# Performance work log

Measured on AMD Instinct MI355X. Metric: run time of the kernel, lower is better.

## Reference

```python
import jax, jax.numpy as jnp
import numpy as np

B, D, H = 16384, 1024, 4096


def setup_inputs() -> dict:
    key = jax.random.key(0)
    kx, kp, k1, k2 = jax.random.split(key, 4)
    X = jax.random.normal(kx, (B, D), dtype=jnp.float32)
    prot_col_idx = 3
    # protected column must be binary {0,1} so the remap produces no NaNs
    prot = jax.random.randint(kp, (B,), 0, 2).astype(jnp.float32)
    X = X.at[:, prot_col_idx].set(prot)
    W1 = jax.random.normal(k1, (D, H), dtype=jnp.float32) * (1.0 / np.sqrt(D))
    b1 = jnp.zeros((H,), dtype=jnp.float32)
    W2 = jax.random.normal(k2, (H, D), dtype=jnp.float32) * (1.0 / np.sqrt(H))
    b2 = jnp.zeros((D,), dtype=jnp.float32)
    return {"X": X, "W1": W1, "b1": b1, "W2": W2, "b2": b2,
            "prot_col_idx": prot_col_idx}


def reference(X, W1, b1, W2, b2, prot_col_idx):
    def explainer(x):
        h = jnp.tanh(x @ W1 + b1)          # [B, H]
        return h @ W2 + b2                  # [B, D]

    # vectorized remap of the protected column: 0 -> 1, 1 -> 0, else NaN
    col = X[:, prot_col_idx]
    flipped = jnp.where(col == 0, jnp.float32(1.0),
                        jnp.where(col == 1, jnp.float32(0.0), jnp.float32(jnp.nan)))
    X_copy = X.at[:, prot_col_idx].set(flipped.astype(X.dtype))

    shaps = explainer(X)
    shaps_counter = explainer(X_copy)
    mean_euclid_dist = jnp.mean(jnp.abs(shaps - shaps_counter), axis=0)  # [D]
    return mean_euclid_dist.sum()
```

## Files before the change

### kernel.cpp

```cpp
#include <hip/hip_runtime.h>
#include <stdint.h>

#define B_N 16384
#define D_N 1024
#define H_N 4096

typedef int i32x4 __attribute__((ext_vector_type(4)));
typedef int i32x8 __attribute__((ext_vector_type(8)));
typedef float f32x4 __attribute__((ext_vector_type(4)));

__device__ __forceinline__ void gload16(const void* g, void* l) {
  __builtin_amdgcn_global_load_lds((const __attribute__((address_space(1))) void*)g,
                                   (__attribute__((address_space(3))) void*)l,
                                   16, 0, 0);
}

__device__ __forceinline__ unsigned char f2fp8(float v) {
  return (unsigned char)(__builtin_amdgcn_cvt_pk_fp8_f32(v, v, 0, false) & 0xFF);
}

__device__ __forceinline__ int perm_h(int h) {
  return (h & ~63) | ((h & 15) << 2) | ((h >> 4) & 3);
}

__device__ __forceinline__ void transpose_tile(
    const float* __restrict__ in, unsigned char* __restrict__ out,
    int R, int C, float scale, float* __restrict__ w3, int pci,
    int i0, int j0, int tx, int ty, bool permute) {
  __shared__ float tile[32][33];
#pragma unroll
  for (int r = 0; r < 32; r += 8) {
    int i = i0 + ty + r;
    int j = j0 + tx;
    float v = in[(size_t)i * C + j];
    tile[ty + r][tx] = v;
    if (w3 != nullptr && i == pci) w3[j] = v;
  }
  __syncthreads();
#pragma unroll
  for (int r = 0; r < 32; r += 8) {
    int jo = j0 + ty + r;
    int io = i0 + tx;
    int ioo = permute ? perm_h(io) : io;
    out[(size_t)jo * R + ioo] = f2fp8(tile[tx][ty + r] * scale);
  }
}

__global__ __launch_bounds__(256) void prep_kernel(
    const float4* __restrict__ X4, int* __restrict__ Xb,
    float* __restrict__ s,
    const float* __restrict__ W1, unsigned char* __restrict__ W1T, float* __restrict__ w3,
    const float* __restrict__ W2, unsigned char* __restrict__ W2T,
    const int* __restrict__ pci_p, float* __restrict__ out0) {
  int b = blockIdx.x;
  int tid = threadIdx.x;
  int pci = *pci_p;
  if (b == 0 && tid == 0) out0[0] = 0.0f;
  if (b < 8192) {
    int i = (b * 256 + tid) * 2;
#pragma unroll
    for (int u = 0; u < 2; u++) {
      float4 v = X4[i + u];
      int p = __builtin_amdgcn_cvt_pk_fp8_f32(v.x, v.y, 0, false);
      p = __builtin_amdgcn_cvt_pk_fp8_f32(v.z, v.w, p, true);
      Xb[i + u] = p;
      if (((i + u) & (D_N / 4 - 1)) == (pci >> 2)) {
        int row = (i + u) >> 8;
        float c;
        switch (pci & 3) {
          case 0:  c = v.x; break;
          case 1:  c = v.y; break;
          case 2:  c = v.z; break;
          default: c = v.w; break;
        }
        s[row] = 1.0f - 2.0f * c;
      }
    }
  } else if (b < 12288) {
    int id = b - 8192;
    transpose_tile(W1, W1T, D_N, H_N, 16.0f, w3, pci,
                   (id >> 7) * 32, (id & 127) * 32, tid & 31, tid >> 5, false);
  } else {
    int id = b - 12288;
    transpose_tile(W2, W2T, H_N, D_N, 64.0f, nullptr, -1,
                   (id >> 5) * 32, (id & 31) * 32, tid & 31, tid >> 5, true);
  }
}

template <int KTOT>
__device__ __forceinline__ void mx_mainloop(
    const unsigned char* __restrict__ A, const unsigned char* __restrict__ B,
    int m0, int n0, int sa, int sb,
    unsigned char* As, unsigned char* Bs, f32x4 (&acc)[4][4]) {
  const int tid = threadIdx.x;
  const int lane = tid & 63;
  const int wave = tid >> 6;
  const int wm = (wave >> 1) * 64;
  const int wn = (wave & 1) * 64;
  const int lm = lane & 15;
  const int quad = lane >> 4;

  const int srow = tid >> 3;
  const int clog = (tid & 7) ^ (srow & 7);
  const unsigned char* Ag = A + (size_t)(m0 + srow) * KTOT + clog * 16;
  const unsigned char* Bg = B + (size_t)(n0 + srow) * KTOT + clog * 16;
  unsigned char* As_l = As + tid * 16;
  unsigned char* Bs_l = Bs + tid * 16;

  for (int k0 = 0; k0 < KTOT; k0 += 128) {
#pragma unroll
    for (int it = 0; it < 4; it++) {
      gload16(Ag + k0 + (size_t)(32 * it) * KTOT, As_l + it * 4096);
      gload16(Bg + k0 + (size_t)(32 * it) * KTOT, Bs_l + it * 4096);
    }
    __syncthreads();
    i32x8 b[4];
#pragma unroll
    for (int j = 0; j < 4; j++) {
      int r = wn + j * 16 + lm;
      int e = r & 7;
      i32x4 lo = *(const i32x4*)&Bs[r * 128 + ((2 * quad) ^ e) * 16];
      i32x4 hi = *(const i32x4*)&Bs[r * 128 + ((2 * quad + 1) ^ e) * 16];
      b[j] = __builtin_shufflevector(lo, hi, 0, 1, 2, 3, 4, 5, 6, 7);
    }
#pragma unroll
    for (int i = 0; i < 4; i++) {
      int r = wm + i * 16 + lm;
      int e = r & 7;
      i32x4 lo = *(const i32x4*)&As[r * 128 + ((2 * quad) ^ e) * 16];
      i32x4 hi = *(const i32x4*)&As[r * 128 + ((2 * quad + 1) ^ e) * 16];
      i32x8 av = __builtin_shufflevector(lo, hi, 0, 1, 2, 3, 4, 5, 6, 7);
#pragma unroll
      for (int j = 0; j < 4; j++)
        acc[i][j] = __builtin_amdgcn_mfma_scale_f32_16x16x128_f8f6f4(
            av, b[j], acc[i][j], 0, 0, 0, sa, 0, sb);
    }
    __syncthreads();
  }
}

__global__ __launch_bounds__(256, 4) void gemm1_dh(
    const unsigned char* __restrict__ Xb,
    const unsigned char* __restrict__ W1T,
    const float* __restrict__ b1,
    const float* __restrict__ w3,
    const float* __restrict__ s,
    unsigned int* __restrict__ Dh4) {
  __shared__ alignas(16) unsigned char As[128 * 128];
  __shared__ alignas(16) unsigned char Bs[128 * 128];
  int l = blockIdx.y * gridDim.x + blockIdx.x;
  int x = l & 7;
  int k = l >> 3;
  int ni = k & 7;
  int m  = (k >> 3) & 15;
  int nc = k >> 7;
  const int m0 = (x * 16 + m) * 128;
  const int n0 = (nc * 8 + ni) * 128;

  f32x4 acc[4][4] = {};
  mx_mainloop<D_N>(Xb, W1T, m0, n0, 127, 123, As, Bs, acc);

  const int tid = threadIdx.x;
  const int lane = tid & 63;
  const int wave = tid >> 6;
  const int wm = (wave >> 1) * 64;
  const int wn = (wave & 1) * 64;
  const int lm = lane & 15;
  const int quad = lane >> 4;

  float ewp[4], ewm[4], nump[4], numm[4], b1v[4];
#pragma unroll
  for (int j = 0; j < 4; j++) {
    int gh = n0 + wn + j * 16 + lm;
    float w = w3[gh];
    float ep = __expf(2.0f * w);
    float em = __expf(-2.0f * w);
    ewp[j] = ep; ewm[j] = em;
    nump[j] = 128.0f * (1.0f - ep);
    numm[j] = 128.0f * (1.0f - em);
    b1v[j] = b1[gh];
  }
  const size_t coloff = (size_t)((n0 + wn) >> 2) + lm;
#pragma unroll
  for (int i = 0; i < 4; i++) {
#pragma unroll
    for (int r = 0; r < 4; r++) {
      int gb = m0 + wm + i * 16 + quad * 4 + r;
      bool sp = s[gb] > 0.0f;
      float o[4];
#pragma unroll
      for (int j = 0; j < 4; j++) {
        float ews = sp ? ewp[j] : ewm[j];
        float num = sp ? nump[j] : numm[j];
        float z = fminf(acc[i][j][r] + b1v[j], 12.0f);
        float E = __expf(2.0f * z);
        float den = (E * ews + 1.0f) * (E + 1.0f);
        o[j] = (E * num) * __builtin_amdgcn_rcpf(den);
      }
      int p = __builtin_amdgcn_cvt_pk_fp8_f32(o[0], o[1], 0, false);
      p = __builtin_amdgcn_cvt_pk_fp8_f32(o[2], o[3], p, true);
      Dh4[(size_t)gb * (H_N / 4) + coloff] = (unsigned int)p;
    }
  }
}

__global__ __launch_bounds__(256, 4) void gemm2_abs(
    const unsigned char* __restrict__ Dh,
    const unsigned char* __restrict__ W2T,
    float* __restrict__ out) {
  __shared__ alignas(16) unsigned char As[128 * 128];
  __shared__ alignas(16) unsigned char Bs[128 * 128];
  __shared__ float wsum[4];
  int l = blockIdx.y * gridDim.x + blockIdx.x;
  int x = l & 7;
  int k = l >> 3;
  int c = k >> 6;
  int idx = k & 63;
  int m  = idx >> 2;
  int nj = idx & 3;
  const int m0 = (x * 16 + m) * 128;
  const int n0 = (c * 4 + nj) * 128;

  f32x4 acc[4][4] = {};
  mx_mainloop<H_N>(Dh, W2T, m0, n0, 121, 121, As, Bs, acc);

  const int tid = threadIdx.x;
  const int lane = tid & 63;
  const int wave = tid >> 6;

  float t = 0.0f;
#pragma unroll
  for (int i = 0; i < 4; i++)
#pragma unroll
    for (int j = 0; j < 4; j++)
#pragma unroll
      for (int r = 0; r < 4; r++)
        t += fabsf(acc[i][j][r]);

#pragma unroll
  for (int off2 = 32; off2 > 0; off2 >>= 1)
    t += __shfl_down(t, off2, 64);
  if (lane == 0) wsum[wave] = t;
  __syncthreads();
  if (tid == 0)
    atomicAdd(out, (wsum[0] + wsum[1] + wsum[2] + wsum[3]) * (1.0f / (float)B_N));
}

extern "C" void kernel_launch(void* const* d_in, const int* in_sizes, int n_in,
                              void* d_out, int out_size, void* d_ws, size_t ws_size,
                              hipStream_t stream) {
  const float* X  = (const float*)d_in[0];
  const float* W1 = (const float*)d_in[1];
  const float* b1 = (const float*)d_in[2];
  const float* W2 = (const float*)d_in[3];
  const int* pci  = (const int*)d_in[5];

  char* ws = (char*)d_ws;
  size_t off = 0;
  unsigned char* Xb  = (unsigned char*)(ws + off); off += (size_t)B_N * D_N;
  unsigned char* W1T = (unsigned char*)(ws + off); off += (size_t)H_N * D_N;
  unsigned char* W2T = (unsigned char*)(ws + off); off += (size_t)D_N * H_N;
  float* w3  = (float*)(ws + off); off += (size_t)H_N * 4;
  float* s   = (float*)(ws + off); off += (size_t)B_N * 4;
  unsigned char* Dh  = (unsigned char*)(ws + off); off += (size_t)B_N * H_N;
  if (ws_size < off) return;

  prep_kernel<<<16384, 256, 0, stream>>>((const float4*)X, (int*)Xb, s,
                                         W1, W1T, w3, W2, W2T, pci,
                                         (float*)d_out);
  gemm1_dh<<<dim3(32, 128), 256, 0, stream>>>(Xb, W1T, b1, w3, s,
                                              (unsigned int*)Dh);
  gemm2_abs<<<dim3(8, 128), 256, 0, stream>>>(Dh, W2T, (float*)d_out);
}
```

Measured before the change: 283.4 us.

## Fuse prep and both GEMMs into one persistent kernel with grid barriers

Replaces three kernel launches with a single persistent kernel of 1024 blocks. The blocks loop over the prep work, then the first GEMM (four N tiles per block) and the second GEMM, separated by atomic-counter grid barriers. The goal is to remove launch gaps and kernel tail effects. In exchange it adds barrier spin cost, a memset launch, and reliance on all 1024 blocks being co-resident (4 per CU); if they are not, the kernel deadlocks. It also changes the tile scheduling order of the first GEMM.

```diff
diff --git a/kernel.cpp b/kernel.cpp
--- a/kernel.cpp
+++ b/kernel.cpp
@@ -23,17 +23,28 @@
   return (h & ~63) | ((h & 15) << 2) | ((h >> 4) & 3);
 }
 
+__device__ __forceinline__ void grid_barrier(int* cnt, int target) {
+  __syncthreads();
+  __threadfence();
+  if (threadIdx.x == 0) {
+    __hip_atomic_fetch_add(cnt, 1, __ATOMIC_RELEASE, __HIP_MEMORY_SCOPE_AGENT);
+    while (__hip_atomic_load(cnt, __ATOMIC_ACQUIRE, __HIP_MEMORY_SCOPE_AGENT) < target)
+      __builtin_amdgcn_s_sleep(8);
+  }
+  __syncthreads();
+  __threadfence();
+}
+
 __device__ __forceinline__ void transpose_tile(
     const float* __restrict__ in, unsigned char* __restrict__ out,
     int R, int C, float scale, float* __restrict__ w3, int pci,
-    int i0, int j0, int tx, int ty, bool permute) {
-  __shared__ float tile[32][33];
+    int i0, int j0, int tx, int ty, bool permute, float* tile ) {
 #pragma unroll
   for (int r = 0; r < 32; r += 8) {
     int i = i0 + ty + r;
     int j = j0 + tx;
     float v = in[(size_t)i * C + j];
-    tile[ty + r][tx] = v;
+    tile[(ty + r) * 33 + tx] = v;
     if (w3 != nullptr && i == pci) w3[j] = v;
   }
   __syncthreads();
@@ -42,49 +53,9 @@
     int jo = j0 + ty + r;
     int io = i0 + tx;
     int ioo = permute ? perm_h(io) : io;
-    out[(size_t)jo * R + ioo] = f2fp8(tile[tx][ty + r] * scale);
-  }
-}
-
-__global__ __launch_bounds__(256) void prep_kernel(
-    const float4* __restrict__ X4, int* __restrict__ Xb,
-    float* __restrict__ s,
-    const float* __restrict__ W1, unsigned char* __restrict__ W1T, float* __restrict__ w3,
-    const float* __restrict__ W2, unsigned char* __restrict__ W2T,
-    const int* __restrict__ pci_p, float* __restrict__ out0) {
-  int b = blockIdx.x;
-  int tid = threadIdx.x;
-  int pci = *pci_p;
-  if (b == 0 && tid == 0) out0[0] = 0.0f;
-  if (b < 8192) {
-    int i = (b * 256 + tid) * 2;
-#pragma unroll
-    for (int u = 0; u < 2; u++) {
-      float4 v = X4[i + u];
-      int p = __builtin_amdgcn_cvt_pk_fp8_f32(v.x, v.y, 0, false);
-      p = __builtin_amdgcn_cvt_pk_fp8_f32(v.z, v.w, p, true);
-      Xb[i + u] = p;
-      if (((i + u) & (D_N / 4 - 1)) == (pci >> 2)) {
-        int row = (i + u) >> 8;
-        float c;
-        switch (pci & 3) {
-          case 0:  c = v.x; break;
-          case 1:  c = v.y; break;
-          case 2:  c = v.z; break;
-          default: c = v.w; break;
-        }
-        s[row] = 1.0f - 2.0f * c;
-      }
-    }
-  } else if (b < 12288) {
-    int id = b - 8192;
-    transpose_tile(W1, W1T, D_N, H_N, 16.0f, w3, pci,
-                   (id >> 7) * 32, (id & 127) * 32, tid & 31, tid >> 5, false);
-  } else {
-    int id = b - 12288;
-    transpose_tile(W2, W2T, H_N, D_N, 64.0f, nullptr, -1,
-                   (id >> 5) * 32, (id & 31) * 32, tid & 31, tid >> 5, true);
-  }
+    out[(size_t)jo * R + ioo] = f2fp8(tile[tx * 33 + ty + r] * scale);
+  }
+  __syncthreads();
 }
 
 template <int KTOT>
@@ -139,111 +110,149 @@
   }
 }
 
-__global__ __launch_bounds__(256, 4) void gemm1_dh(
-    const unsigned char* __restrict__ Xb,
-    const unsigned char* __restrict__ W1T,
-    const float* __restrict__ b1,
-    const float* __restrict__ w3,
-    const float* __restrict__ s,
-    unsigned int* __restrict__ Dh4) {
-  __shared__ alignas(16) unsigned char As[128 * 128];
-  __shared__ alignas(16) unsigned char Bs[128 * 128];
-  int l = blockIdx.y * gridDim.x + blockIdx.x;
-  int x = l & 7;
-  int k = l >> 3;
-  int ni = k & 7;
-  int m  = (k >> 3) & 15;
-  int nc = k >> 7;
-  const int m0 = (x * 16 + m) * 128;
-  const int n0 = (nc * 8 + ni) * 128;
-
-  f32x4 acc[4][4] = {};
-  mx_mainloop<D_N>(Xb, W1T, m0, n0, 127, 123, As, Bs, acc);
-
-  const int tid = threadIdx.x;
-  const int lane = tid & 63;
-  const int wave = tid >> 6;
-  const int wm = (wave >> 1) * 64;
-  const int wn = (wave & 1) * 64;
-  const int lm = lane & 15;
-  const int quad = lane >> 4;
-
-  float ewp[4], ewm[4], nump[4], numm[4], b1v[4];
-#pragma unroll
-  for (int j = 0; j < 4; j++) {
-    int gh = n0 + wn + j * 16 + lm;
-    float w = w3[gh];
-    float ep = __expf(2.0f * w);
-    float em = __expf(-2.0f * w);
-    ewp[j] = ep; ewm[j] = em;
-    nump[j] = 128.0f * (1.0f - ep);
-    numm[j] = 128.0f * (1.0f - em);
-    b1v[j] = b1[gh];
-  }
-  const size_t coloff = (size_t)((n0 + wn) >> 2) + lm;
-#pragma unroll
-  for (int i = 0; i < 4; i++) {
-#pragma unroll
-    for (int r = 0; r < 4; r++) {
-      int gb = m0 + wm + i * 16 + quad * 4 + r;
-      bool sp = s[gb] > 0.0f;
-      float o[4];
-#pragma unroll
-      for (int j = 0; j < 4; j++) {
-        float ews = sp ? ewp[j] : ewm[j];
-        float num = sp ? nump[j] : numm[j];
-        float z = fminf(acc[i][j][r] + b1v[j], 12.0f);
-        float E = __expf(2.0f * z);
-        float den = (E * ews + 1.0f) * (E + 1.0f);
-        o[j] = (E * num) * __builtin_amdgcn_rcpf(den);
-      }
-      int p = __builtin_amdgcn_cvt_pk_fp8_f32(o[0], o[1], 0, false);
-      p = __builtin_amdgcn_cvt_pk_fp8_f32(o[2], o[3], p, true);
-      Dh4[(size_t)gb * (H_N / 4) + coloff] = (unsigned int)p;
-    }
-  }
-}
-
-__global__ __launch_bounds__(256, 4) void gemm2_abs(
-    const unsigned char* __restrict__ Dh,
-    const unsigned char* __restrict__ W2T,
+__global__ __launch_bounds__(256, 4) void fused_kernel(
+    const float4* __restrict__ X4, unsigned char* __restrict__ Xb,
+    float* __restrict__ s,
+    const float* __restrict__ W1, unsigned char* __restrict__ W1T,
+    float* __restrict__ w3,
+    const float* __restrict__ W2, unsigned char* __restrict__ W2T,
+    const int* __restrict__ pci_p, const float* __restrict__ b1,
+    unsigned char* __restrict__ Dh, int* __restrict__ bar,
     float* __restrict__ out) {
   __shared__ alignas(16) unsigned char As[128 * 128];
   __shared__ alignas(16) unsigned char Bs[128 * 128];
   __shared__ float wsum[4];
-  int l = blockIdx.y * gridDim.x + blockIdx.x;
-  int x = l & 7;
-  int k = l >> 3;
-  int c = k >> 6;
-  int idx = k & 63;
-  int m  = idx >> 2;
-  int nj = idx & 3;
-  const int m0 = (x * 16 + m) * 128;
-  const int n0 = (c * 4 + nj) * 128;
-
-  f32x4 acc[4][4] = {};
-  mx_mainloop<H_N>(Dh, W2T, m0, n0, 121, 121, As, Bs, acc);
-
+
+  const int bid = blockIdx.x;
   const int tid = threadIdx.x;
-  const int lane = tid & 63;
-  const int wave = tid >> 6;
-
-  float t = 0.0f;
-#pragma unroll
-  for (int i = 0; i < 4; i++)
-#pragma unroll
-    for (int j = 0; j < 4; j++)
-#pragma unroll
-      for (int r = 0; r < 4; r++)
-        t += fabsf(acc[i][j][r]);
-
-#pragma unroll
-  for (int off2 = 32; off2 > 0; off2 >>= 1)
-    t += __shfl_down(t, off2, 64);
-  if (lane == 0) wsum[wave] = t;
-  __syncthreads();
-  if (tid == 0)
-    atomicAdd(out, (wsum[0] + wsum[1] + wsum[2] + wsum[3]) * (1.0f / (float)B_N));
+  const int pci = *pci_p;
+
+  if (bid == 0 && tid == 0)
+    __hip_atomic_store(out, 0.0f, __ATOMIC_RELAXED, __HIP_MEMORY_SCOPE_AGENT);
+#pragma unroll 1
+  for (int u = 0; u < 16; u++) {
+    int vb = u * 1024 + bid;
+    if (vb < 8192) {
+      int i = (vb * 256 + tid) * 2;
+#pragma unroll
+      for (int v2 = 0; v2 < 2; v2++) {
+        float4 v = X4[i + v2];
+        int p = __builtin_amdgcn_cvt_pk_fp8_f32(v.x, v.y, 0, false);
+        p = __builtin_amdgcn_cvt_pk_fp8_f32(v.z, v.w, p, true);
+        ((int*)Xb)[i + v2] = p;
+        if (((i + v2) & (D_N / 4 - 1)) == (pci >> 2)) {
+          int row = (i + v2) >> 8;
+          float c;
+          switch (pci & 3) {
+            case 0:  c = v.x; break;
+            case 1:  c = v.y; break;
+            case 2:  c = v.z; break;
+            default: c = v.w; break;
+          }
+          s[row] = 1.0f - 2.0f * c;
+        }
+      }
+    } else if (vb < 12288) {
+      int id = vb - 8192;
+      transpose_tile(W1, W1T, D_N, H_N, 16.0f, w3, pci,
+                     (id >> 7) * 32, (id & 127) * 32, tid & 31, tid >> 5,
+                     false, (float*)As);
+    } else {
+      int id = vb - 12288;
+      transpose_tile(W2, W2T, H_N, D_N, 64.0f, nullptr, -1,
+                     (id >> 5) * 32, (id & 31) * 32, tid & 31, tid >> 5,
+                     true, (float*)As);
+    }
+  }
+  grid_barrier(bar, 1024);
+
+  {
+    const int x = bid & 7;
+    const int ni = (bid >> 3) & 7;
+    const int m = bid >> 6;
+    const int m0 = (x * 16 + m) * 128;
+    const int lane = tid & 63;
+    const int wave = tid >> 6;
+    const int wm = (wave >> 1) * 64;
+    const int wn = (wave & 1) * 64;
+    const int lm = lane & 15;
+    const int quad = lane >> 4;
+#pragma unroll 1
+    for (int nc = 0; nc < 4; nc++) {
+      const int n0 = (nc * 8 + ni) * 128;
+      f32x4 acc[4][4] = {};
+      mx_mainloop<D_N>(Xb, W1T, m0, n0, 127, 123, As, Bs, acc);
+
+      float ewp[4], ewm[4], nump[4], numm[4], b1v[4];
+#pragma unroll
+      for (int j = 0; j < 4; j++) {
+        int gh = n0 + wn + j * 16 + lm;
+        float w = w3[gh];
+        float ep = __expf(2.0f * w);
+        float em = __expf(-2.0f * w);
+        ewp[j] = ep; ewm[j] = em;
+        nump[j] = 128.0f * (1.0f - ep);
+        numm[j] = 128.0f * (1.0f - em);
+        b1v[j] = b1[gh];
+      }
+      const size_t coloff = (size_t)((n0 + wn) >> 2) + lm;
+#pragma unroll
+      for (int i = 0; i < 4; i++) {
+#pragma unroll
+        for (int r = 0; r < 4; r++) {
+          int gb = m0 + wm + i * 16 + quad * 4 + r;
+          bool sp = s[gb] > 0.0f;
+          float o[4];
+#pragma unroll
+          for (int j = 0; j < 4; j++) {
+            float ews = sp ? ewp[j] : ewm[j];
+            float num = sp ? nump[j] : numm[j];
+            float z = fminf(acc[i][j][r] + b1v[j], 12.0f);
+            float E = __expf(2.0f * z);
+            float den = (E * ews + 1.0f) * (E + 1.0f);
+            o[j] = (E * num) * __builtin_amdgcn_rcpf(den);
+          }
+          int p = __builtin_amdgcn_cvt_pk_fp8_f32(o[0], o[1], 0, false);
+          p = __builtin_amdgcn_cvt_pk_fp8_f32(o[2], o[3], p, true);
+          ((unsigned int*)Dh)[(size_t)gb * (H_N / 4) + coloff] = (unsigned int)p;
+        }
+      }
+    }
+  }
+  grid_barrier(bar, 2048);
+
+  {
+    const int x = bid & 7;
+    const int k = bid >> 3;
+    const int c = k >> 6;
+    const int idx = k & 63;
+    const int m = idx >> 2;
+    const int nj = idx & 3;
+    const int m0 = (x * 16 + m) * 128;
+    const int n0 = (c * 4 + nj) * 128;
+
+    f32x4 acc[4][4] = {};
+    mx_mainloop<H_N>(Dh, W2T, m0, n0, 121, 121, As, Bs, acc);
+
+    const int lane = tid & 63;
+    const int wave = tid >> 6;
+    float t = 0.0f;
+#pragma unroll
+    for (int i = 0; i < 4; i++)
+#pragma unroll
+      for (int j = 0; j < 4; j++)
+#pragma unroll
+        for (int r = 0; r < 4; r++)
+          t += fabsf(acc[i][j][r]);
+
+#pragma unroll
+    for (int off2 = 32; off2 > 0; off2 >>= 1)
+      t += __shfl_down(t, off2, 64);
+    if (lane == 0) wsum[wave] = t;
+    __syncthreads();
+    if (tid == 0)
+      atomicAdd(out, (wsum[0] + wsum[1] + wsum[2] + wsum[3]) * (1.0f / (float)B_N));
+  }
 }
 
 extern "C" void kernel_launch(void* const* d_in, const int* in_sizes, int n_in,
@@ -263,12 +272,11 @@
   float* w3  = (float*)(ws + off); off += (size_t)H_N * 4;
   float* s   = (float*)(ws + off); off += (size_t)B_N * 4;
   unsigned char* Dh  = (unsigned char*)(ws + off); off += (size_t)B_N * H_N;
+  int* bar = (int*)(ws + off); off += 256;
   if (ws_size < off) return;
 
-  prep_kernel<<<16384, 256, 0, stream>>>((const float4*)X, (int*)Xb, s,
-                                         W1, W1T, w3, W2, W2T, pci,
-                                         (float*)d_out);
-  gemm1_dh<<<dim3(32, 128), 256, 0, stream>>>(Xb, W1T, b1, w3, s,
-                                              (unsigned int*)Dh);
-  gemm2_abs<<<dim3(8, 128), 256, 0, stream>>>(Dh, W2T, (float*)d_out);
-}
+  hipMemsetAsync(bar, 0, sizeof(int), stream);
+  fused_kernel<<<1024, 256, 0, stream>>>(
+      (const float4*)X, Xb, s, W1, W1T, w3, W2, W2T, pci, b1, Dh, bar,
+      (float*)d_out);
+}
```

After: 993.8 us. 251% more time.

## Fuse both GEMMs into one persistent kernel with per-panel counters

Applied to the files above, without the earlier changes.

Merges the two GEMM launches into one 1024-block kernel. Each block computes four GEMM1 tiles, stages the fp8 results in LDS and writes them with coalesced nontemporal 16-byte stores, then bumps a per-row-panel atomic counter. Each block's GEMM2 tile spin-waits until its panel's counter reaches 32 before running. This lets GEMM2 on finished panels overlap with GEMM1 still running elsewhere and removes a launch boundary. The cost is fewer blocks for GEMM1, extra LDS staging and syncs, and a risk of deadlock if not all blocks are co-resident.

```diff
diff --git a/kernel.cpp b/kernel.cpp
--- a/kernel.cpp
+++ b/kernel.cpp
@@ -8,6 +8,7 @@
 typedef int i32x4 __attribute__((ext_vector_type(4)));
 typedef int i32x8 __attribute__((ext_vector_type(8)));
 typedef float f32x4 __attribute__((ext_vector_type(4)));
+typedef unsigned int u32x4 __attribute__((ext_vector_type(4)));
 
 __device__ __forceinline__ void gload16(const void* g, void* l) {
   __builtin_amdgcn_global_load_lds((const __attribute__((address_space(1))) void*)g,
@@ -49,13 +50,18 @@
 __global__ __launch_bounds__(256) void prep_kernel(
     const float4* __restrict__ X4, int* __restrict__ Xb,
     float* __restrict__ s,
-    const float* __restrict__ W1, unsigned char* __restrict__ W1T, float* __restrict__ w3,
+    const float* __restrict__ W1, unsigned char* __restrict__ W1T,
+    float* __restrict__ w3,
     const float* __restrict__ W2, unsigned char* __restrict__ W2T,
-    const int* __restrict__ pci_p, float* __restrict__ out0) {
+    const int* __restrict__ pci_p, int* __restrict__ cnt,
+    float* __restrict__ out0) {
   int b = blockIdx.x;
   int tid = threadIdx.x;
   int pci = *pci_p;
-  if (b == 0 && tid == 0) out0[0] = 0.0f;
+  if (b == 0) {
+    if (tid < 128) cnt[tid] = 0;
+    if (tid == 0) out0[0] = 0.0f;
+  }
   if (b < 8192) {
     int i = (b * 256 + tid) * 2;
 #pragma unroll
@@ -139,27 +145,23 @@
   }
 }
 
-__global__ __launch_bounds__(256, 4) void gemm1_dh(
+__global__ __launch_bounds__(256, 4) void fused_gemm(
     const unsigned char* __restrict__ Xb,
     const unsigned char* __restrict__ W1T,
     const float* __restrict__ b1,
     const float* __restrict__ w3,
     const float* __restrict__ s,
-    unsigned int* __restrict__ Dh4) {
-  __shared__ alignas(16) unsigned char As[128 * 128];
-  __shared__ alignas(16) unsigned char Bs[128 * 128];
-  int l = blockIdx.y * gridDim.x + blockIdx.x;
-  int x = l & 7;
-  int k = l >> 3;
-  int ni = k & 7;
-  int m  = (k >> 3) & 15;
-  int nc = k >> 7;
-  const int m0 = (x * 16 + m) * 128;
-  const int n0 = (nc * 8 + ni) * 128;
-
-  f32x4 acc[4][4] = {};
-  mx_mainloop<D_N>(Xb, W1T, m0, n0, 127, 123, As, Bs, acc);
-
+    unsigned char* __restrict__ Dh,
+    const unsigned char* __restrict__ W2T,
+    int* __restrict__ cnt,
+    float* __restrict__ out) {
+  __shared__ alignas(16) unsigned char smem[32768];
+  __shared__ float wsum[4];
+  unsigned char* As = smem;
+  unsigned char* Bs = smem + 16384;
+  unsigned int* stage = (unsigned int*)smem;
+
+  const int bid = blockIdx.x;
   const int tid = threadIdx.x;
   const int lane = tid & 63;
   const int wave = tid >> 6;
@@ -168,82 +170,105 @@
   const int lm = lane & 15;
   const int quad = lane >> 4;
 
-  float ewp[4], ewm[4], nump[4], numm[4], b1v[4];
-#pragma unroll
-  for (int j = 0; j < 4; j++) {
-    int gh = n0 + wn + j * 16 + lm;
-    float w = w3[gh];
-    float ep = __expf(2.0f * w);
-    float em = __expf(-2.0f * w);
-    ewp[j] = ep; ewm[j] = em;
-    nump[j] = 128.0f * (1.0f - ep);
-    numm[j] = 128.0f * (1.0f - em);
-    b1v[j] = b1[gh];
-  }
-  const size_t coloff = (size_t)((n0 + wn) >> 2) + lm;
-#pragma unroll
-  for (int i = 0; i < 4; i++) {
-#pragma unroll
-    for (int r = 0; r < 4; r++) {
-      int gb = m0 + wm + i * 16 + quad * 4 + r;
-      bool sp = s[gb] > 0.0f;
-      float o[4];
+  {
+    const int x = bid & 7;
+    const int ni = (bid >> 3) & 7;
+    const int m = bid >> 6;
+    const int m0 = (x * 16 + m) * 128;
+    const int panel = x * 16 + m;
+#pragma unroll 1
+    for (int nc = 0; nc < 4; nc++) {
+      const int n0 = (nc * 8 + ni) * 128;
+      f32x4 acc[4][4] = {};
+      mx_mainloop<D_N>(Xb, W1T, m0, n0, 127, 123, As, Bs, acc);
+
+      float ewp[4], ewm[4], nump[4], numm[4], b1v[4];
 #pragma unroll
       for (int j = 0; j < 4; j++) {
-        float ews = sp ? ewp[j] : ewm[j];
-        float num = sp ? nump[j] : numm[j];
-        float z = fminf(acc[i][j][r] + b1v[j], 12.0f);
-        float E = __expf(2.0f * z);
-        float den = (E * ews + 1.0f) * (E + 1.0f);
-        o[j] = (E * num) * __builtin_amdgcn_rcpf(den);
-      }
-      int p = __builtin_amdgcn_cvt_pk_fp8_f32(o[0], o[1], 0, false);
-      p = __builtin_amdgcn_cvt_pk_fp8_f32(o[2], o[3], p, true);
-      Dh4[(size_t)gb * (H_N / 4) + coloff] = (unsigned int)p;
-    }
-  }
-}
-
-__global__ __launch_bounds__(256, 4) void gemm2_abs(
-    const unsigned char* __restrict__ Dh,
-    const unsigned char* __restrict__ W2T,
-    float* __restrict__ out) {
-  __shared__ alignas(16) unsigned char As[128 * 128];
-  __shared__ alignas(16) unsigned char Bs[128 * 128];
-  __shared__ float wsum[4];
-  int l = blockIdx.y * gridDim.x + blockIdx.x;
-  int x = l & 7;
-  int k = l >> 3;
-  int c = k >> 6;
-  int idx = k & 63;
-  int m  = idx >> 2;
-  int nj = idx & 3;
-  const int m0 = (x * 16 + m) * 128;
-  const int n0 = (c * 4 + nj) * 128;
-
-  f32x4 acc[4][4] = {};
-  mx_mainloop<H_N>(Dh, W2T, m0, n0, 121, 121, As, Bs, acc);
-
-  const int tid = threadIdx.x;
-  const int lane = tid & 63;
-  const int wave = tid >> 6;
-
-  float t = 0.0f;
-#pragma unroll
-  for (int i = 0; i < 4; i++)
-#pragma unroll
-    for (int j = 0; j < 4; j++)
-#pragma unroll
-      for (int r = 0; r < 4; r++)
-        t += fabsf(acc[i][j][r]);
-
-#pragma unroll
-  for (int off2 = 32; off2 > 0; off2 >>= 1)
-    t += __shfl_down(t, off2, 64);
-  if (lane == 0) wsum[wave] = t;
-  __syncthreads();
-  if (tid == 0)
-    atomicAdd(out, (wsum[0] + wsum[1] + wsum[2] + wsum[3]) * (1.0f / (float)B_N));
+        int gh = n0 + wn + j * 16 + lm;
+        float w = w3[gh];
+        float ep = __expf(2.0f * w);
+        float em = __expf(-2.0f * w);
+        ewp[j] = ep; ewm[j] = em;
+        nump[j] = 128.0f * (1.0f - ep);
+        numm[j] = 128.0f * (1.0f - em);
+        b1v[j] = b1[gh];
+      }
+      const int scol = ((wn >> 2) & 31) + lm;
+#pragma unroll
+      for (int i = 0; i < 4; i++) {
+#pragma unroll
+        for (int r = 0; r < 4; r++) {
+          int trow = wm + i * 16 + quad * 4 + r;
+          bool sp = s[m0 + trow] > 0.0f;
+          float o[4];
+#pragma unroll
+          for (int j = 0; j < 4; j++) {
+            float ews = sp ? ewp[j] : ewm[j];
+            float num = sp ? nump[j] : numm[j];
+            float z = fminf(acc[i][j][r] + b1v[j], 12.0f);
+            float E = __expf(2.0f * z);
+            float den = (E * ews + 1.0f) * (E + 1.0f);
+            o[j] = (E * num) * __builtin_amdgcn_rcpf(den);
+          }
+          int p = __builtin_amdgcn_cvt_pk_fp8_f32(o[0], o[1], 0, false);
+          p = __builtin_amdgcn_cvt_pk_fp8_f32(o[2], o[3], p, true);
+          stage[trow * 36 + scol] = (unsigned int)p;
+        }
+      }
+      __syncthreads();
+#pragma unroll
+      for (int w = 0; w < 4; w++) {
+        int idx = tid + 256 * w;
+        int row = idx >> 3, c = idx & 7;
+        u32x4 v = *(const u32x4*)(stage + row * 36 + 4 * c);
+        __builtin_nontemporal_store(
+            v, (u32x4*)Dh + (size_t)(m0 + row) * 256 + (n0 >> 4) + c);
+      }
+      __syncthreads();
+      if (tid == 0)
+        __hip_atomic_fetch_add(&cnt[panel], 1, __ATOMIC_RELAXED,
+                               __HIP_MEMORY_SCOPE_AGENT);
+    }
+  }
+
+  {
+    const int x = bid & 7;
+    const int k = bid >> 3;
+    const int c = k >> 6;
+    const int idx = k & 63;
+    const int m = idx >> 2;
+    const int nj = idx & 3;
+    const int m0 = (x * 16 + m) * 128;
+    const int n0 = (c * 4 + nj) * 128;
+    const int panel = x * 16 + m;
+
+    if (tid == 0)
+      while (__hip_atomic_load(&cnt[panel], __ATOMIC_RELAXED,
+                               __HIP_MEMORY_SCOPE_AGENT) < 32)
+        __builtin_amdgcn_s_sleep(2);
+    __syncthreads();
+
+    f32x4 acc[4][4] = {};
+    mx_mainloop<H_N>(Dh, W2T, m0, n0, 121, 121, As, Bs, acc);
+
+    float t = 0.0f;
+#pragma unroll
+    for (int i = 0; i < 4; i++)
+#pragma unroll
+      for (int j = 0; j < 4; j++)
+#pragma unroll
+        for (int r = 0; r < 4; r++)
+          t += fabsf(acc[i][j][r]);
+
+#pragma unroll
+    for (int off2 = 32; off2 > 0; off2 >>= 1)
+      t += __shfl_down(t, off2, 64);
+    if (lane == 0) wsum[wave] = t;
+    __syncthreads();
+    if (tid == 0)
+      atomicAdd(out, (wsum[0] + wsum[1] + wsum[2] + wsum[3]) * (1.0f / (float)B_N));
+  }
 }
 
 extern "C" void kernel_launch(void* const* d_in, const int* in_sizes, int n_in,
@@ -263,12 +288,12 @@
   float* w3  = (float*)(ws + off); off += (size_t)H_N * 4;
   float* s   = (float*)(ws + off); off += (size_t)B_N * 4;
   unsigned char* Dh  = (unsigned char*)(ws + off); off += (size_t)B_N * H_N;
+  int* cnt = (int*)(ws + off); off += 512;
   if (ws_size < off) return;
 
   prep_kernel<<<16384, 256, 0, stream>>>((const float4*)X, (int*)Xb, s,
-                                         W1, W1T, w3, W2, W2T, pci,
+                                         W1, W1T, w3, W2, W2T, pci, cnt,
                                          (float*)d_out);
-  gemm1_dh<<<dim3(32, 128), 256, 0, stream>>>(Xb, W1T, b1, w3, s,
-                                              (unsigned int*)Dh);
-  gemm2_abs<<<dim3(8, 128), 256, 0, stream>>>(Dh, W2T, (float*)d_out);
-}
+  fused_gemm<<<1024, 256, 0, stream>>>(Xb, W1T, b1, w3, s, Dh, W2T, cnt,
+                                       (float*)d_out);
+}
```

After: 360.3 us. 1.27x slower.
